# Kernel optimization log

Measured on AMD Instinct MI355X. Metric: run time of the kernel, lower is better.

Reference implementation:

```python
import jax, jax.numpy as jnp
import numpy as np

NUM_NODES = 100000
NUM_EDGES = 1600000
EMB, HID, IN = 32, 64, 128


def gcn_conv(x, W, b, src, dst, n):
    # PyG GCNConv: add self-loops, symmetric normalization, linear transform, sum-aggregate, bias.
    h = x @ W                                   # [n, out]
    deg = jnp.zeros((n,), x.dtype).at[dst].add(1.0) + 1.0  # degree incl. self-loop
    dinv = jax.lax.rsqrt(deg)                   # deg^{-1/2}
    norm = dinv[src] * dinv[dst]                # [E]
    msg = h[src] * norm[:, None]                # gather + scale  [E, out]
    agg = jax.ops.segment_sum(msg, dst, num_segments=n)
    agg = agg + h * (dinv * dinv)[:, None]      # self-loop contribution
    return agg + b


def setup_inputs() -> dict:
    key = jax.random.key(0)
    ks = jax.random.split(key, 10)
    f32 = jnp.float32
    edge_index = jax.random.randint(ks[0], (2, NUM_EDGES), 0, NUM_NODES, dtype=jnp.int64 if jax.config.jax_enable_x64 else jnp.int32)
    def glorot(k, fan_in, fan_out):
        s = (6.0 / (fan_in + fan_out)) ** 0.5
        return jax.random.uniform(k, (fan_in, fan_out), f32, -s, s)
    return {
        'edge_index': edge_index,
        'embedding': jax.random.normal(ks[1], (NUM_NODES, EMB), f32),
        'We1': glorot(ks[2], EMB, HID), 'be1': jnp.zeros((HID,), f32),
        'We2': glorot(ks[3], HID, EMB), 'be2': jnp.zeros((EMB,), f32),
        'Wd1': glorot(ks[4], EMB, HID), 'bd1': jnp.zeros((HID,), f32),
        'Wd2': glorot(ks[5], HID, IN),  'bd2': jnp.zeros((IN,), f32),
    }


def reference(edge_index, embedding, We1, be1, We2, be2, Wd1, bd1, Wd2, bd2):
    src, dst = edge_index[0], edge_index[1]
    n = NUM_NODES
    # encoder
    x = jax.nn.relu(gcn_conv(embedding, We1, be1, src, dst, n))
    z = jax.nn.relu(gcn_conv(x, We2, be2, src, dst, n))
    # decoder
    y = jax.nn.relu(gcn_conv(z, Wd1, bd1, src, dst, n))
    recon_x = gcn_conv(y, Wd2, bd2, src, dst, n)
    return (recon_x, z)
```

## Files before the change

### kernel.cpp

```cpp
#include <hip/hip_runtime.h>
#include <hip/hip_fp16.h>

#define NN 100000
#define NE 1600000
#define NB 782
#define EPB 2048
#define NBLK_A 782
#define SCNT (NB * NBLK_A)
#define SC_NB ((SCNT + 1023) / 1024)
#define CAP 4096


__global__ void bhistA_kernel(const int* __restrict__ dst, int* __restrict__ histT) {
    __shared__ int hist[NB];
    int t = threadIdx.x, b = blockIdx.x;
    for (int i = t; i < NB; i += 256) hist[i] = 0;
    __syncthreads();
    int e0 = b * EPB + t * 4;
#pragma unroll
    for (int half = 0; half < 2; ++half) {
        int e = e0 + half * 1024;
        if (e < NE) {
            int4 d4 = *(const int4*)(dst + e);
            atomicAdd(&hist[d4.x >> 7], 1);
            atomicAdd(&hist[d4.y >> 7], 1);
            atomicAdd(&hist[d4.z >> 7], 1);
            atomicAdd(&hist[d4.w >> 7], 1);
        }
    }
    __syncthreads();
    for (int i = t; i < NB; i += 256) histT[i * NBLK_A + b] = hist[i];
}

__global__ void scan1g_kernel(const int* __restrict__ in, int* __restrict__ out,
                              int* __restrict__ blkSum) {
    __shared__ int ts[256];
    int t = threadIdx.x, b = blockIdx.x;
    int base = b * 1024 + t * 4;
    int4 c = {0, 0, 0, 0};
    if (base < SCNT) c = *(const int4*)(in + base);
    int s = c.x + c.y + c.z + c.w;
    ts[t] = s;
    __syncthreads();
    for (int ofs = 1; ofs < 256; ofs <<= 1) {
        int v = (t >= ofs) ? ts[t - ofs] : 0;
        __syncthreads();
        ts[t] += v;
        __syncthreads();
    }
    if (t == 255) blkSum[b] = ts[255];
    int ex = ts[t] - s;
    if (base < SCNT) {
        int4 p;
        p.x = ex; p.y = ex + c.x; p.z = p.y + c.y; p.w = p.z + c.z;
        *(int4*)(out + base) = p;
    }
}

__global__ void scan2g_kernel(int* __restrict__ blkSum) {
    __shared__ int ts[1024];
    int t = threadIdx.x;
    int v = (t < SC_NB) ? blkSum[t] : 0;
    ts[t] = v;
    __syncthreads();
    for (int ofs = 1; ofs < 1024; ofs <<= 1) {
        int u = (t >= ofs) ? ts[t - ofs] : 0;
        __syncthreads();
        ts[t] += u;
        __syncthreads();
    }
    if (t < SC_NB) blkSum[t] = ts[t] - v;
}

__global__ void bscatB_kernel(const int* __restrict__ src, const int* __restrict__ dst,
                              const int* __restrict__ scanT, const int* __restrict__ blkSum,
                              int* __restrict__ ebuf) {
    __shared__ int cur[NB];
    int t = threadIdx.x, b = blockIdx.x;
    for (int i = t; i < NB; i += 256) {
        int idx = i * NBLK_A + b;
        cur[i] = scanT[idx] + blkSum[idx >> 10];
    }
    __syncthreads();
    int e0 = b * EPB + t * 4;
#pragma unroll
    for (int half = 0; half < 2; ++half) {
        int e = e0 + half * 1024;
        if (e < NE) {
            int4 d4 = *(const int4*)(dst + e);
            int4 s4 = *(const int4*)(src + e);
            int p0 = atomicAdd(&cur[d4.x >> 7], 1);
            ebuf[p0] = s4.x | ((d4.x & 127) << 20);
            int p1 = atomicAdd(&cur[d4.y >> 7], 1);
            ebuf[p1] = s4.y | ((d4.y & 127) << 20);
            int p2 = atomicAdd(&cur[d4.z >> 7], 1);
            ebuf[p2] = s4.z | ((d4.z & 127) << 20);
            int p3 = atomicAdd(&cur[d4.w >> 7], 1);
            ebuf[p3] = s4.w | ((d4.w & 127) << 20);
        }
    }
}

__global__ void csrC_kernel(const int* __restrict__ ebuf, const int* __restrict__ scanT,
                            const int* __restrict__ blkSum,
                            int* __restrict__ row_ptr, int* __restrict__ col,
                            float* __restrict__ dinv) {
    __shared__ int es[CAP];
    __shared__ int hist[128];
    __shared__ int ts[128];
    __shared__ int cur[128];
    int t = threadIdx.x, b = blockIdx.x;
    int i0 = b * NBLK_A;
    int base = scanT[i0] + blkSum[i0 >> 10];
    int end;
    if (b + 1 < NB) {
        int i1 = (b + 1) * NBLK_A;
        end = scanT[i1] + blkSum[i1 >> 10];
    } else {
        end = NE;
    }
    int cnt = end - base;
    if (t < 128) hist[t] = 0;
    __syncthreads();
    for (int i = t; i < cnt; i += 256) {
        int e = ebuf[base + i];
        if (i < CAP) es[i] = e;
        atomicAdd(&hist[e >> 20], 1);
    }
    __syncthreads();
    if (t < 128) ts[t] = hist[t];
    __syncthreads();
    for (int ofs = 1; ofs < 128; ofs <<= 1) {
        int v = 0;
        if (t < 128 && t >= ofs) v = ts[t - ofs];
        __syncthreads();
        if (t < 128) ts[t] += v;
        __syncthreads();
    }
    if (t < 128) {
        int ex = ts[t] - hist[t];
        cur[t] = ex;
        int g = b * 128 + t;
        if (g < NN) {
            row_ptr[g] = base + ex;
            dinv[g] = rsqrtf((float)hist[t] + 1.0f);
        }
    }
    if (b == 0 && t == 0) row_ptr[NN] = NE;
    __syncthreads();
    for (int i = t; i < cnt; i += 256) {
        int e = (i < CAP) ? es[i] : ebuf[base + i];
        int r = atomicAdd(&cur[e >> 20], 1);
        col[base + r] = e & 0xFFFFF;
    }
}


__device__ inline ushort4 f4_to_h4(float4 v) {
    ushort4 o;
    o.x = __half_as_ushort(__float2half(v.x));
    o.y = __half_as_ushort(__float2half(v.y));
    o.z = __half_as_ushort(__float2half(v.z));
    o.w = __half_as_ushort(__float2half(v.w));
    return o;
}

template<int C>
__global__ void quant_kernel(const float4* __restrict__ x, const float* __restrict__ dinv,
                             ushort4* __restrict__ q) {
    constexpr int TPN = C / 4;
    int gid = blockIdx.x * blockDim.x + threadIdx.x;
    if (gid >= NN * TPN) return;
    int node = gid / TPN;
    float d = dinv[node];
    float4 v = x[gid];
    v.x *= d; v.y *= d; v.z *= d; v.w *= d;
    q[gid] = f4_to_h4(v);
}

template<int IN, int OUT, bool RELU, bool HASBIAS, bool QUANT>
__global__ void mm_kernel(const float* __restrict__ x, const float* __restrict__ W,
                          const float* __restrict__ bias, const float* __restrict__ dinv,
                          float4* __restrict__ out, ushort4* __restrict__ qout) {
    constexpr int CG   = OUT / 4;
    constexpr int RG   = 256 / CG;
    constexpr int ROWS = RG * 4;
    constexpr int P    = IN + 4;
    __shared__ float4 Ws[IN * CG];
    __shared__ float  xs[ROWS * P];

    int tid = threadIdx.x;
    const float4* W4 = (const float4*)W;
    for (int i = tid; i < IN * CG; i += 256) Ws[i] = W4[i];

    int n0 = blockIdx.x * ROWS;
    for (int i = tid; i < ROWS * IN; i += 256) {
        int r = i / IN, c = i & (IN - 1);
        size_t g = (size_t)n0 * IN + i;
        if (g < (size_t)NN * IN) xs[r * P + c] = x[g];
    }
    __syncthreads();

    int cg = tid % CG;
    int rg = tid / CG;

    float4 acc[4] = {{0,0,0,0},{0,0,0,0},{0,0,0,0},{0,0,0,0}};
#pragma unroll 2
    for (int k = 0; k < IN; k += 4) {
        float4 w0 = Ws[(k + 0) * CG + cg];
        float4 w1 = Ws[(k + 1) * CG + cg];
        float4 w2 = Ws[(k + 2) * CG + cg];
        float4 w3 = Ws[(k + 3) * CG + cg];
#pragma unroll
        for (int i = 0; i < 4; ++i) {
            float4 xq = *(const float4*)&xs[(i * RG + rg) * P + k];
            acc[i].x = fmaf(xq.x, w0.x, acc[i].x);
            acc[i].y = fmaf(xq.x, w0.y, acc[i].y);
            acc[i].z = fmaf(xq.x, w0.z, acc[i].z);
            acc[i].w = fmaf(xq.x, w0.w, acc[i].w);
            acc[i].x = fmaf(xq.y, w1.x, acc[i].x);
            acc[i].y = fmaf(xq.y, w1.y, acc[i].y);
            acc[i].z = fmaf(xq.y, w1.z, acc[i].z);
            acc[i].w = fmaf(xq.y, w1.w, acc[i].w);
            acc[i].x = fmaf(xq.z, w2.x, acc[i].x);
            acc[i].y = fmaf(xq.z, w2.y, acc[i].y);
            acc[i].z = fmaf(xq.z, w2.z, acc[i].z);
            acc[i].w = fmaf(xq.z, w2.w, acc[i].w);
            acc[i].x = fmaf(xq.w, w3.x, acc[i].x);
            acc[i].y = fmaf(xq.w, w3.y, acc[i].y);
            acc[i].z = fmaf(xq.w, w3.z, acc[i].z);
            acc[i].w = fmaf(xq.w, w3.w, acc[i].w);
        }
    }

    float4 bb = {0, 0, 0, 0};
    if (HASBIAS) bb = ((const float4*)bias)[cg];
#pragma unroll
    for (int i = 0; i < 4; ++i) {
        int node = n0 + i * RG + rg;
        if (node >= NN) continue;
        float4 r = acc[i];
        if (HASBIAS) { r.x += bb.x; r.y += bb.y; r.z += bb.z; r.w += bb.w; }
        if (RELU) {
            r.x = fmaxf(r.x, 0.f); r.y = fmaxf(r.y, 0.f);
            r.z = fmaxf(r.z, 0.f); r.w = fmaxf(r.w, 0.f);
        }
        if (QUANT) {
            float d = dinv[node];
            r.x *= d; r.y *= d; r.z *= d; r.w *= d;
            qout[(size_t)node * CG + cg] = f4_to_h4(r);
        } else {
            out[(size_t)node * CG + cg] = r;
        }
    }
}


__device__ inline void acc8(float* a, uint4 u) {
    const __half2* hp = (const __half2*)&u;
#pragma unroll
    for (int q = 0; q < 4; ++q) {
        float2 f = __half22float2(hp[q]);
        a[2 * q]     += f.x;
        a[2 * q + 1] += f.y;
    }
}

template<int C, bool BIASRELU, bool WRITE_Q>
__global__ void agg_kernel(const uint4* __restrict__ h, const int* __restrict__ row_ptr,
                           const int* __restrict__ col, const float* __restrict__ dinv,
                           const float* __restrict__ b, float4* __restrict__ out,
                           uint4* __restrict__ qout) {
    constexpr int TPN = C / 8;
    int gid = blockIdx.x * blockDim.x + threadIdx.x;
    int node = gid / TPN;
    int cg = gid % TPN;
    if (node >= NN) return;
    int beg = row_ptr[node];
    int end = row_ptr[node + 1];

    float a[8] = {0, 0, 0, 0, 0, 0, 0, 0};
    acc8(a, h[(size_t)node * TPN + cg]);

    int j = beg;
    for (; j < end && (j & 3); ++j) acc8(a, h[(size_t)col[j] * TPN + cg]);
    for (; j + 8 <= end; j += 8) {
        int4 c0 = *(const int4*)(col + j);
        int4 c1 = *(const int4*)(col + j + 4);
        uint4 u0 = h[(size_t)c0.x * TPN + cg];
        uint4 u1 = h[(size_t)c0.y * TPN + cg];
        uint4 u2 = h[(size_t)c0.z * TPN + cg];
        uint4 u3 = h[(size_t)c0.w * TPN + cg];
        uint4 u4 = h[(size_t)c1.x * TPN + cg];
        uint4 u5 = h[(size_t)c1.y * TPN + cg];
        uint4 u6 = h[(size_t)c1.z * TPN + cg];
        uint4 u7 = h[(size_t)c1.w * TPN + cg];
        acc8(a, u0); acc8(a, u1); acc8(a, u2); acc8(a, u3);
        acc8(a, u4); acc8(a, u5); acc8(a, u6); acc8(a, u7);
    }
    for (; j + 4 <= end; j += 4) {
        int4 c0 = *(const int4*)(col + j);
        uint4 u0 = h[(size_t)c0.x * TPN + cg];
        uint4 u1 = h[(size_t)c0.y * TPN + cg];
        uint4 u2 = h[(size_t)c0.z * TPN + cg];
        uint4 u3 = h[(size_t)c0.w * TPN + cg];
        acc8(a, u0); acc8(a, u1); acc8(a, u2); acc8(a, u3);
    }
    for (; j < end; ++j) acc8(a, h[(size_t)col[j] * TPN + cg]);

    float d = dinv[node];
    float r[8];
    if (BIASRELU) {
        const float* bp = b + cg * 8;
#pragma unroll
        for (int q = 0; q < 8; ++q) r[q] = fmaxf(fmaf(d, a[q], bp[q]), 0.f);
    } else {
#pragma unroll
        for (int q = 0; q < 8; ++q) r[q] = d * a[q];
    }
    float4* op = out + (size_t)node * (C / 4) + cg * 2;
    op[0] = make_float4(r[0], r[1], r[2], r[3]);
    op[1] = make_float4(r[4], r[5], r[6], r[7]);
    if (WRITE_Q) {
        uint4 qv;
        __half2* qp = (__half2*)&qv;
#pragma unroll
        for (int q = 0; q < 4; ++q)
            qp[q] = __float22half2_rn(make_float2(r[2 * q] * d, r[2 * q + 1] * d));
        qout[(size_t)node * TPN + cg] = qv;
    }
}


extern "C" void kernel_launch(void* const* d_in, const int* in_sizes, int n_in,
                              void* d_out, int out_size, void* d_ws, size_t ws_size,
                              hipStream_t stream) {
    const int* ei = (const int*)d_in[0];
    const int* src = ei;
    const int* dst = ei + NE;
    const float* emb = (const float*)d_in[1];
    const float* We1 = (const float*)d_in[2]; const float* be1 = (const float*)d_in[3];
    const float* We2 = (const float*)d_in[4]; const float* be2 = (const float*)d_in[5];
    const float* Wd1 = (const float*)d_in[6]; const float* bd1 = (const float*)d_in[7];
    const float* Wd2 = (const float*)d_in[8]; const float* bd2 = (const float*)d_in[9];

    float* outp  = (float*)d_out;
    float* recon = outp;
    float* z     = outp + (size_t)NN * 128;

    char* ws = (char*)d_ws;
    size_t off = 0;
    auto alloc = [&](size_t bytes) {
        void* p = ws + off;
        off += (bytes + 255) & ~(size_t)255;
        return p;
    };
    int*     row_ptr = (int*)    alloc((size_t)(NN + 1) * 4);
    int*     col     = (int*)    alloc((size_t)NE * 4);
    float*   dinv    = (float*)  alloc((size_t)NN * 4);
    int*     histT   = (int*)    alloc((size_t)SCNT * 4);
    int*     scanT   = (int*)    alloc((size_t)SCNT * 4);
    int*     blkSum  = (int*)    alloc((size_t)SC_NB * 4);
    void*    region1 = alloc((size_t)NN * 32 * 4);
    ushort4* qA      = (ushort4*)alloc((size_t)NN * 64 * 2);
    ushort4* qB      = (ushort4*)alloc((size_t)NN * 64 * 2);
    float*   fB      = (float*)  alloc((size_t)NN * 64 * 4);
    int*     ebuf    = (int*)region1;
    float*   fA      = (float*)region1;
    (void)ws_size; (void)in_sizes; (void)n_in; (void)out_size;

    bhistA_kernel<<<NBLK_A, 256, 0, stream>>>(dst, histT);
    scan1g_kernel<<<SC_NB, 256, 0, stream>>>(histT, scanT, blkSum);
    scan2g_kernel<<<1, 1024, 0, stream>>>(blkSum);
    bscatB_kernel<<<NBLK_A, 256, 0, stream>>>(src, dst, scanT, blkSum, ebuf);
    csrC_kernel<<<NB, 256, 0, stream>>>(ebuf, scanT, blkSum, row_ptr, col, dinv);

    quant_kernel<32><<<(NN * 8 + 255) / 256, 256, 0, stream>>>((const float4*)emb, dinv, qA);
    agg_kernel<32, false, false><<<(NN * 4 + 255) / 256, 256, 0, stream>>>(
        (const uint4*)qA, row_ptr, col, dinv, nullptr, (float4*)fA, nullptr);
    mm_kernel<32, 64, true, true, false><<<(NN + 63) / 64, 256, 0, stream>>>(
        fA, We1, be1, dinv, (float4*)fB, nullptr);

    mm_kernel<64, 32, false, false, true><<<(NN + 127) / 128, 256, 0, stream>>>(
        fB, We2, nullptr, dinv, nullptr, qB);
    agg_kernel<32, true, true><<<(NN * 4 + 255) / 256, 256, 0, stream>>>(
        (const uint4*)qB, row_ptr, col, dinv, be2, (float4*)z, (uint4*)qA);

    agg_kernel<32, false, false><<<(NN * 4 + 255) / 256, 256, 0, stream>>>(
        (const uint4*)qA, row_ptr, col, dinv, nullptr, (float4*)fA, nullptr);
    mm_kernel<32, 64, true, true, true><<<(NN + 63) / 64, 256, 0, stream>>>(
        fA, Wd1, bd1, dinv, nullptr, qB);

    agg_kernel<64, false, false><<<(NN * 8 + 255) / 256, 256, 0, stream>>>(
        (const uint4*)qB, row_ptr, col, dinv, nullptr, (float4*)fB, nullptr);
    mm_kernel<64, 128, false, true, false><<<(NN + 31) / 32, 256, 0, stream>>>(
        fB, Wd2, bd2, dinv, (float4*)recon, nullptr);
}
```

Baseline: 261.9 us.

## Fuse aggregation into matmul kernels and fold embedding quantization into CSR build

Adds an aggmm kernel that gathers neighbor features into shared memory and immediately multiplies by the weight, removing the float intermediate round trip and a kernel launch for three of the layers. Embedding scaling and fp16 quantization move into the tail of the CSR-building kernel, using the per-block dinv kept in shared memory. The ebuf buffer no longer aliases the fp32 intermediate. The fused kernel ties the aggregation thread layout to the matmul tile, and there are fewer gather threads per block than in the standalone aggregation kernel, which may reduce memory-level parallelism.

```diff
diff --git a/kernel.cpp b/kernel.cpp
--- a/kernel.cpp
+++ b/kernel.cpp
@@ -101,14 +101,26 @@
     }
 }
 
+
+__device__ inline ushort4 f4_to_h4(float4 v) {
+    ushort4 o;
+    o.x = __half_as_ushort(__float2half(v.x));
+    o.y = __half_as_ushort(__float2half(v.y));
+    o.z = __half_as_ushort(__float2half(v.z));
+    o.w = __half_as_ushort(__float2half(v.w));
+    return o;
+}
+
 __global__ void csrC_kernel(const int* __restrict__ ebuf, const int* __restrict__ scanT,
                             const int* __restrict__ blkSum,
                             int* __restrict__ row_ptr, int* __restrict__ col,
-                            float* __restrict__ dinv) {
+                            float* __restrict__ dinv,
+                            const float4* __restrict__ emb, ushort4* __restrict__ qA) {
     __shared__ int es[CAP];
     __shared__ int hist[128];
     __shared__ int ts[128];
     __shared__ int cur[128];
+    __shared__ float dl[128];
     int t = threadIdx.x, b = blockIdx.x;
     int i0 = b * NBLK_A;
     int base = scanT[i0] + blkSum[i0 >> 10];
@@ -140,10 +152,12 @@
     if (t < 128) {
         int ex = ts[t] - hist[t];
         cur[t] = ex;
+        float dv = rsqrtf((float)hist[t] + 1.0f);
+        dl[t] = dv;
         int g = b * 128 + t;
         if (g < NN) {
             row_ptr[g] = base + ex;
-            dinv[g] = rsqrtf((float)hist[t] + 1.0f);
+            dinv[g] = dv;
         }
     }
     if (b == 0 && t == 0) row_ptr[NN] = NE;
@@ -153,29 +167,93 @@
         int r = atomicAdd(&cur[e >> 20], 1);
         col[base + r] = e & 0xFFFFF;
     }
-}
-
-
-__device__ inline ushort4 f4_to_h4(float4 v) {
-    ushort4 o;
-    o.x = __half_as_ushort(__float2half(v.x));
-    o.y = __half_as_ushort(__float2half(v.y));
-    o.z = __half_as_ushort(__float2half(v.z));
-    o.w = __half_as_ushort(__float2half(v.w));
-    return o;
-}
-
-template<int C>
-__global__ void quant_kernel(const float4* __restrict__ x, const float* __restrict__ dinv,
-                             ushort4* __restrict__ q) {
-    constexpr int TPN = C / 4;
+    for (int i = t; i < 128 * 8; i += 256) {
+        int ln = i >> 3;
+        int g = b * 128 + ln;
+        if (g < NN) {
+            float4 v = emb[(size_t)g * 8 + (i & 7)];
+            float d = dl[ln];
+            v.x *= d; v.y *= d; v.z *= d; v.w *= d;
+            qA[(size_t)g * 8 + (i & 7)] = f4_to_h4(v);
+        }
+    }
+}
+
+
+__device__ inline void acc8(float* a, uint4 u) {
+    const __half2* hp = (const __half2*)&u;
+#pragma unroll
+    for (int q = 0; q < 4; ++q) {
+        float2 f = __half22float2(hp[q]);
+        a[2 * q]     += f.x;
+        a[2 * q + 1] += f.y;
+    }
+}
+
+template<int TPN>
+__device__ inline void agg_node(float* a, const uint4* __restrict__ h,
+                                const int* __restrict__ col, int node, int beg, int end, int cg) {
+    acc8(a, h[(size_t)node * TPN + cg]);
+    int j = beg;
+    for (; j < end && (j & 3); ++j) acc8(a, h[(size_t)col[j] * TPN + cg]);
+    for (; j + 8 <= end; j += 8) {
+        int4 c0 = *(const int4*)(col + j);
+        int4 c1 = *(const int4*)(col + j + 4);
+        uint4 u0 = h[(size_t)c0.x * TPN + cg];
+        uint4 u1 = h[(size_t)c0.y * TPN + cg];
+        uint4 u2 = h[(size_t)c0.z * TPN + cg];
+        uint4 u3 = h[(size_t)c0.w * TPN + cg];
+        uint4 u4 = h[(size_t)c1.x * TPN + cg];
+        uint4 u5 = h[(size_t)c1.y * TPN + cg];
+        uint4 u6 = h[(size_t)c1.z * TPN + cg];
+        uint4 u7 = h[(size_t)c1.w * TPN + cg];
+        acc8(a, u0); acc8(a, u1); acc8(a, u2); acc8(a, u3);
+        acc8(a, u4); acc8(a, u5); acc8(a, u6); acc8(a, u7);
+    }
+    for (; j + 4 <= end; j += 4) {
+        int4 c0 = *(const int4*)(col + j);
+        uint4 u0 = h[(size_t)c0.x * TPN + cg];
+        uint4 u1 = h[(size_t)c0.y * TPN + cg];
+        uint4 u2 = h[(size_t)c0.z * TPN + cg];
+        uint4 u3 = h[(size_t)c0.w * TPN + cg];
+        acc8(a, u0); acc8(a, u1); acc8(a, u2); acc8(a, u3);
+    }
+    for (; j < end; ++j) acc8(a, h[(size_t)col[j] * TPN + cg]);
+}
+
+template<int C, bool BIASRELU, bool WRITE_Q>
+__global__ void agg_kernel(const uint4* __restrict__ h, const int* __restrict__ row_ptr,
+                           const int* __restrict__ col, const float* __restrict__ dinv,
+                           const float* __restrict__ b, float4* __restrict__ out,
+                           uint4* __restrict__ qout) {
+    constexpr int TPN = C / 8;
     int gid = blockIdx.x * blockDim.x + threadIdx.x;
-    if (gid >= NN * TPN) return;
     int node = gid / TPN;
+    int cg = gid % TPN;
+    if (node >= NN) return;
+    float a[8] = {0, 0, 0, 0, 0, 0, 0, 0};
+    agg_node<TPN>(a, h, col, node, row_ptr[node], row_ptr[node + 1], cg);
     float d = dinv[node];
-    float4 v = x[gid];
-    v.x *= d; v.y *= d; v.z *= d; v.w *= d;
-    q[gid] = f4_to_h4(v);
+    float r[8];
+    if (BIASRELU) {
+        const float* bp = b + cg * 8;
+#pragma unroll
+        for (int q = 0; q < 8; ++q) r[q] = fmaxf(fmaf(d, a[q], bp[q]), 0.f);
+    } else {
+#pragma unroll
+        for (int q = 0; q < 8; ++q) r[q] = d * a[q];
+    }
+    float4* op = out + (size_t)node * (C / 4) + cg * 2;
+    op[0] = make_float4(r[0], r[1], r[2], r[3]);
+    op[1] = make_float4(r[4], r[5], r[6], r[7]);
+    if (WRITE_Q) {
+        uint4 qv;
+        __half2* qp = (__half2*)&qv;
+#pragma unroll
+        for (int q = 0; q < 4; ++q)
+            qp[q] = __float22half2_rn(make_float2(r[2 * q] * d, r[2 * q + 1] * d));
+        qout[(size_t)node * TPN + cg] = qv;
+    }
 }
 
 template<int IN, int OUT, bool RELU, bool HASBIAS, bool QUANT>
@@ -255,79 +333,94 @@
     }
 }
 
-
-__device__ inline void acc8(float* a, uint4 u) {
-    const __half2* hp = (const __half2*)&u;
-#pragma unroll
-    for (int q = 0; q < 4; ++q) {
-        float2 f = __half22float2(hp[q]);
-        a[2 * q]     += f.x;
-        a[2 * q + 1] += f.y;
-    }
-}
-
-template<int C, bool BIASRELU, bool WRITE_Q>
-__global__ void agg_kernel(const uint4* __restrict__ h, const int* __restrict__ row_ptr,
-                           const int* __restrict__ col, const float* __restrict__ dinv,
-                           const float* __restrict__ b, float4* __restrict__ out,
-                           uint4* __restrict__ qout) {
-    constexpr int TPN = C / 8;
-    int gid = blockIdx.x * blockDim.x + threadIdx.x;
-    int node = gid / TPN;
-    int cg = gid % TPN;
-    if (node >= NN) return;
-    int beg = row_ptr[node];
-    int end = row_ptr[node + 1];
-
-    float a[8] = {0, 0, 0, 0, 0, 0, 0, 0};
-    acc8(a, h[(size_t)node * TPN + cg]);
-
-    int j = beg;
-    for (; j < end && (j & 3); ++j) acc8(a, h[(size_t)col[j] * TPN + cg]);
-    for (; j + 8 <= end; j += 8) {
-        int4 c0 = *(const int4*)(col + j);
-        int4 c1 = *(const int4*)(col + j + 4);
-        uint4 u0 = h[(size_t)c0.x * TPN + cg];
-        uint4 u1 = h[(size_t)c0.y * TPN + cg];
-        uint4 u2 = h[(size_t)c0.z * TPN + cg];
-        uint4 u3 = h[(size_t)c0.w * TPN + cg];
-        uint4 u4 = h[(size_t)c1.x * TPN + cg];
-        uint4 u5 = h[(size_t)c1.y * TPN + cg];
-        uint4 u6 = h[(size_t)c1.z * TPN + cg];
-        uint4 u7 = h[(size_t)c1.w * TPN + cg];
-        acc8(a, u0); acc8(a, u1); acc8(a, u2); acc8(a, u3);
-        acc8(a, u4); acc8(a, u5); acc8(a, u6); acc8(a, u7);
-    }
-    for (; j + 4 <= end; j += 4) {
-        int4 c0 = *(const int4*)(col + j);
-        uint4 u0 = h[(size_t)c0.x * TPN + cg];
-        uint4 u1 = h[(size_t)c0.y * TPN + cg];
-        uint4 u2 = h[(size_t)c0.z * TPN + cg];
-        uint4 u3 = h[(size_t)c0.w * TPN + cg];
-        acc8(a, u0); acc8(a, u1); acc8(a, u2); acc8(a, u3);
-    }
-    for (; j < end; ++j) acc8(a, h[(size_t)col[j] * TPN + cg]);
-
-    float d = dinv[node];
-    float r[8];
-    if (BIASRELU) {
-        const float* bp = b + cg * 8;
-#pragma unroll
-        for (int q = 0; q < 8; ++q) r[q] = fmaxf(fmaf(d, a[q], bp[q]), 0.f);
-    } else {
-#pragma unroll
-        for (int q = 0; q < 8; ++q) r[q] = d * a[q];
-    }
-    float4* op = out + (size_t)node * (C / 4) + cg * 2;
-    op[0] = make_float4(r[0], r[1], r[2], r[3]);
-    op[1] = make_float4(r[4], r[5], r[6], r[7]);
-    if (WRITE_Q) {
-        uint4 qv;
-        __half2* qp = (__half2*)&qv;
-#pragma unroll
-        for (int q = 0; q < 4; ++q)
-            qp[q] = __float22half2_rn(make_float2(r[2 * q] * d, r[2 * q + 1] * d));
-        qout[(size_t)node * TPN + cg] = qv;
+template<int IN, int OUT, bool RELU, bool HASBIAS, bool QUANT>
+__global__ void aggmm_kernel(const uint4* __restrict__ h, const int* __restrict__ row_ptr,
+                             const int* __restrict__ col, const float* __restrict__ dinv,
+                             const float* __restrict__ W, const float* __restrict__ bias,
+                             float4* __restrict__ out, ushort4* __restrict__ qout) {
+    constexpr int CG    = OUT / 4;
+    constexpr int RG    = 256 / CG;
+    constexpr int ROWS  = RG * 4;
+    constexpr int P     = IN + 4;
+    constexpr int TPN_A = IN / 8;
+    static_assert(ROWS * TPN_A == 256, "agg/mm decomposition mismatch");
+    __shared__ float4 Ws[IN * CG];
+    __shared__ float  xs[ROWS * P];
+
+    int tid = threadIdx.x;
+    const float4* W4 = (const float4*)W;
+    for (int i = tid; i < IN * CG; i += 256) Ws[i] = W4[i];
+
+    int n0 = blockIdx.x * ROWS;
+
+    {
+        int ln = tid / TPN_A;
+        int cg = tid % TPN_A;
+        int node = n0 + ln;
+        float a[8] = {0, 0, 0, 0, 0, 0, 0, 0};
+        if (node < NN) {
+            agg_node<TPN_A>(a, h, col, node, row_ptr[node], row_ptr[node + 1], cg);
+            float d = dinv[node];
+#pragma unroll
+            for (int q = 0; q < 8; ++q) a[q] *= d;
+        }
+        float* xp = &xs[ln * P + cg * 8];
+        *(float4*)xp       = make_float4(a[0], a[1], a[2], a[3]);
+        *(float4*)(xp + 4) = make_float4(a[4], a[5], a[6], a[7]);
+    }
+    __syncthreads();
+
+    int cg = tid % CG;
+    int rg = tid / CG;
+
+    float4 acc[4] = {{0,0,0,0},{0,0,0,0},{0,0,0,0},{0,0,0,0}};
+#pragma unroll 2
+    for (int k = 0; k < IN; k += 4) {
+        float4 w0 = Ws[(k + 0) * CG + cg];
+        float4 w1 = Ws[(k + 1) * CG + cg];
+        float4 w2 = Ws[(k + 2) * CG + cg];
+        float4 w3 = Ws[(k + 3) * CG + cg];
+#pragma unroll
+        for (int i = 0; i < 4; ++i) {
+            float4 xq = *(const float4*)&xs[(i * RG + rg) * P + k];
+            acc[i].x = fmaf(xq.x, w0.x, acc[i].x);
+            acc[i].y = fmaf(xq.x, w0.y, acc[i].y);
+            acc[i].z = fmaf(xq.x, w0.z, acc[i].z);
+            acc[i].w = fmaf(xq.x, w0.w, acc[i].w);
+            acc[i].x = fmaf(xq.y, w1.x, acc[i].x);
+            acc[i].y = fmaf(xq.y, w1.y, acc[i].y);
+            acc[i].z = fmaf(xq.y, w1.z, acc[i].z);
+            acc[i].w = fmaf(xq.y, w1.w, acc[i].w);
+            acc[i].x = fmaf(xq.z, w2.x, acc[i].x);
+            acc[i].y = fmaf(xq.z, w2.y, acc[i].y);
+            acc[i].z = fmaf(xq.z, w2.z, acc[i].z);
+            acc[i].w = fmaf(xq.z, w2.w, acc[i].w);
+            acc[i].x = fmaf(xq.w, w3.x, acc[i].x);
+            acc[i].y = fmaf(xq.w, w3.y, acc[i].y);
+            acc[i].z = fmaf(xq.w, w3.z, acc[i].z);
+            acc[i].w = fmaf(xq.w, w3.w, acc[i].w);
+        }
+    }
+
+    float4 bb = {0, 0, 0, 0};
+    if (HASBIAS) bb = ((const float4*)bias)[cg];
+#pragma unroll
+    for (int i = 0; i < 4; ++i) {
+        int node = n0 + i * RG + rg;
+        if (node >= NN) continue;
+        float4 r = acc[i];
+        if (HASBIAS) { r.x += bb.x; r.y += bb.y; r.z += bb.z; r.w += bb.w; }
+        if (RELU) {
+            r.x = fmaxf(r.x, 0.f); r.y = fmaxf(r.y, 0.f);
+            r.z = fmaxf(r.z, 0.f); r.w = fmaxf(r.w, 0.f);
+        }
+        if (QUANT) {
+            float d = dinv[node];
+            r.x *= d; r.y *= d; r.z *= d; r.w *= d;
+            qout[(size_t)node * CG + cg] = f4_to_h4(r);
+        } else {
+            out[(size_t)node * CG + cg] = r;
+        }
     }
 }
 
@@ -361,38 +454,30 @@
     int*     histT   = (int*)    alloc((size_t)SCNT * 4);
     int*     scanT   = (int*)    alloc((size_t)SCNT * 4);
     int*     blkSum  = (int*)    alloc((size_t)SC_NB * 4);
-    void*    region1 = alloc((size_t)NN * 32 * 4);
+    int*     ebuf    = (int*)    alloc((size_t)NE * 4);
     ushort4* qA      = (ushort4*)alloc((size_t)NN * 64 * 2);
     ushort4* qB      = (ushort4*)alloc((size_t)NN * 64 * 2);
     float*   fB      = (float*)  alloc((size_t)NN * 64 * 4);
-    int*     ebuf    = (int*)region1;
-    float*   fA      = (float*)region1;
     (void)ws_size; (void)in_sizes; (void)n_in; (void)out_size;
 
     bhistA_kernel<<<NBLK_A, 256, 0, stream>>>(dst, histT);
     scan1g_kernel<<<SC_NB, 256, 0, stream>>>(histT, scanT, blkSum);
     scan2g_kernel<<<1, 1024, 0, stream>>>(blkSum);
     bscatB_kernel<<<NBLK_A, 256, 0, stream>>>(src, dst, scanT, blkSum, ebuf);
-    csrC_kernel<<<NB, 256, 0, stream>>>(ebuf, scanT, blkSum, row_ptr, col, dinv);
-
-    quant_kernel<32><<<(NN * 8 + 255) / 256, 256, 0, stream>>>((const float4*)emb, dinv, qA);
-    agg_kernel<32, false, false><<<(NN * 4 + 255) / 256, 256, 0, stream>>>(
-        (const uint4*)qA, row_ptr, col, dinv, nullptr, (float4*)fA, nullptr);
-    mm_kernel<32, 64, true, true, false><<<(NN + 63) / 64, 256, 0, stream>>>(
-        fA, We1, be1, dinv, (float4*)fB, nullptr);
+    csrC_kernel<<<NB, 256, 0, stream>>>(ebuf, scanT, blkSum, row_ptr, col, dinv,
+                                        (const float4*)emb, qA);
+
+    aggmm_kernel<32, 64, true, true, false><<<(NN + 63) / 64, 256, 0, stream>>>(
+        (const uint4*)qA, row_ptr, col, dinv, We1, be1, (float4*)fB, nullptr);
 
     mm_kernel<64, 32, false, false, true><<<(NN + 127) / 128, 256, 0, stream>>>(
         fB, We2, nullptr, dinv, nullptr, qB);
     agg_kernel<32, true, true><<<(NN * 4 + 255) / 256, 256, 0, stream>>>(
         (const uint4*)qB, row_ptr, col, dinv, be2, (float4*)z, (uint4*)qA);
 
-    agg_kernel<32, false, false><<<(NN * 4 + 255) / 256, 256, 0, stream>>>(
-        (const uint4*)qA, row_ptr, col, dinv, nullptr, (float4*)fA, nullptr);
-    mm_kernel<32, 64, true, true, true><<<(NN + 63) / 64, 256, 0, stream>>>(
-        fA, Wd1, bd1, dinv, nullptr, qB);
-
-    agg_kernel<64, false, false><<<(NN * 8 + 255) / 256, 256, 0, stream>>>(
-        (const uint4*)qB, row_ptr, col, dinv, nullptr, (float4*)fB, nullptr);
-    mm_kernel<64, 128, false, true, false><<<(NN + 31) / 32, 256, 0, stream>>>(
-        fB, Wd2, bd2, dinv, (float4*)recon, nullptr);
-}
+    aggmm_kernel<32, 64, true, true, true><<<(NN + 63) / 64, 256, 0, stream>>>(
+        (const uint4*)qA, row_ptr, col, dinv, Wd1, bd1, nullptr, (ushort4*)qB);
+
+    aggmm_kernel<64, 128, false, true, false><<<(NN + 31) / 32, 256, 0, stream>>>(
+        (const uint4*)qB, row_ptr, col, dinv, Wd2, bd2, (float4*)recon, nullptr);
+}
```

Measured after the change: 237.2 us. 9.4% less time.
